# Kernel tuning notes

Measured on AMD Instinct MI355X. Metric: run time of the kernel, lower is better.

Reference implementation:

```python
import jax, jax.numpy as jnp
import numpy as np

N, E, D, H, K = 8192, 8, 1024, 4096, 2


def setup_inputs() -> dict:
    key = jax.random.key(0)
    ks = jax.random.split(key, 12)
    s = 0.02  # init scale for weights
    return {
        "x": jax.random.normal(ks[0], (N, D), jnp.float32),
        "noise": jax.random.normal(ks[1], (N, E), jnp.float32),
        "Wg_w": jax.random.normal(ks[2], (D, E), jnp.float32) * s,
        "Wg_b": jnp.zeros((E,), jnp.float32),
        "Wn_w": jax.random.normal(ks[3], (D, E), jnp.float32) * s,
        "Wn_b": jnp.zeros((E,), jnp.float32),
        "w1": jax.random.normal(ks[4], (E, D, H), jnp.float32) * s,
        "b1": jnp.zeros((E, H), jnp.float32),
        "w2": jax.random.normal(ks[5], (E, H, D), jnp.float32) * s,
        "b2": jnp.zeros((E, D), jnp.float32),
        "k": K,
    }


def reference(x, noise, Wg_w, Wg_b, Wn_w, Wn_b, w1, b1, w2, b2, k):
    # --- noisy top-k gating: H(x) = Wg(x) + noise * softplus(Wn(x)) ---
    g_logits = x @ Wg_w + Wg_b                       # [N, E]
    n_scale = jax.nn.softplus(x @ Wn_w + Wn_b)       # [N, E]
    h = g_logits + noise * n_scale                   # [N, E]
    topk_vals, topk_inds = jax.lax.top_k(h, k)       # [N, k]
    gates = jax.nn.softmax(topk_vals, axis=-1)       # [N, k]

    # Scatter top-k gates into a dense [N, E] map (zeros for unselected experts),
    # so the weighted combine is exactly sum_j gates[n,j] * expert_{inds[n,j]}(x_n).
    n_tok, n_exp = h.shape
    dense_gates = jnp.zeros((n_tok, n_exp), h.dtype).at[
        jnp.arange(n_tok)[:, None], topk_inds
    ].set(gates)                                     # [N, E]

    # --- per-expert 2-layer MLP: fc2(relu(fc1(x))) ---
    hid = jax.nn.relu(jnp.einsum('nd,edh->neh', x, w1) + b1)  # [N, E, H]
    y = jnp.einsum('neh,ehd->ned', hid, w2) + b2              # [N, E, D]
    out = jnp.einsum('ned,ne->nd', y, dense_gates)            # [N, D]
    return out
```

## Files before the change

### kernel.cpp

```cpp
#include <hip/hip_runtime.h>
#include <hip/hip_bf16.h>

#define NTOK 8192
#define NEXP 8
#define DMODEL 1024
#define DHID 4096

typedef __bf16 bf16x8 __attribute__((ext_vector_type(8)));
typedef float f32x4 __attribute__((ext_vector_type(4)));

__device__ __forceinline__ unsigned short f2bf(float f) {
  return __builtin_bit_cast(unsigned short, __float2bfloat16(f));
}

__device__ __forceinline__ void gload_lds16(const void* g, void* l) {
  __builtin_amdgcn_global_load_lds(
      (const __attribute__((address_space(1))) unsigned int*)g,
      (__attribute__((address_space(3))) unsigned int*)l, 16, 0, 0);
}

__device__ __forceinline__ int imin(int a, int b) { return a < b ? a : b; }

constexpr size_t OFF_XB   = 0;
constexpr size_t OFF_W1T  = OFF_XB + (size_t)NTOK * DMODEL * 2;
constexpr size_t OFF_W2T  = OFF_W1T + (size_t)NEXP * DHID * DMODEL * 2;
constexpr size_t OFF_HID  = OFF_W2T + (size_t)NEXP * DMODEL * DHID * 2;
constexpr size_t OFF_IDX  = OFF_HID + (size_t)NTOK * 2 * DHID * 2;
constexpr size_t OFF_GATE = OFF_IDX + (size_t)NTOK * 2 * 4;
constexpr size_t OFF_LIST = OFF_GATE + (size_t)NTOK * 2 * 4;
constexpr size_t OFF_CNT  = OFF_LIST + (size_t)NTOK * 2 * 4;
constexpr size_t OFF_OFFS = OFF_CNT + 128;
constexpr size_t OFF_CUR  = OFF_OFFS + 128;

__global__ __launch_bounds__(256) void prep_kernel(
    const float* __restrict__ w1, const float* __restrict__ w2,
    unsigned short* __restrict__ w1t, unsigned short* __restrict__ w2t,
    const float* __restrict__ x, const float* __restrict__ noise,
    const float* __restrict__ Wg_w, const float* __restrict__ Wg_b,
    const float* __restrict__ Wn_w, const float* __restrict__ Wn_b,
    unsigned short* __restrict__ xb, int* __restrict__ topk_idx,
    float* __restrict__ topk_gate, int* __restrict__ counts) {
  __shared__ float sh[64][65];
  const int bid = blockIdx.x;

  if (bid < 16384) {
    const float* in;
    unsigned short* outp;
    int R, C, r0, c0;
    if (bid < 8192) {
      int e = bid >> 10, rem = bid & 1023;
      R = DMODEL; C = DHID;
      in = w1 + (size_t)e * R * C;
      outp = w1t + (size_t)e * R * C;
      r0 = (rem >> 6) * 64;
      c0 = (rem & 63) * 64;
    } else {
      int t = bid - 8192;
      int e = t >> 10, rem = t & 1023;
      R = DHID; C = DMODEL;
      in = w2 + (size_t)e * R * C;
      outp = w2t + (size_t)e * R * C;
      r0 = (rem >> 4) * 64;
      c0 = (rem & 15) * 64;
    }
    int tx = threadIdx.x & 15, ty = threadIdx.x >> 4;
#pragma unroll
    for (int p = 0; p < 4; ++p) {
      int row = ty + p * 16;
      float4 v = *(const float4*)&in[(size_t)(r0 + row) * C + c0 + tx * 4];
      sh[row][tx * 4 + 0] = v.x;
      sh[row][tx * 4 + 1] = v.y;
      sh[row][tx * 4 + 2] = v.z;
      sh[row][tx * 4 + 3] = v.w;
    }
    __syncthreads();
#pragma unroll
    for (int p = 0; p < 4; ++p) {
      int crow = ty + p * 16;
      ushort4 o;
      o.x = f2bf(sh[tx * 4 + 0][crow]);
      o.y = f2bf(sh[tx * 4 + 1][crow]);
      o.z = f2bf(sh[tx * 4 + 2][crow]);
      o.w = f2bf(sh[tx * 4 + 3][crow]);
      *(ushort4*)&outp[(size_t)(c0 + crow) * R + r0 + tx * 4] = o;
    }
    return;
  }

  int g = bid - 16384;
  int wave = threadIdx.x >> 6;
  int lane = threadIdx.x & 63;
  int n = g * 4 + wave;
  if (n >= NTOK) return;

  float ag[8] = {0.f, 0.f, 0.f, 0.f, 0.f, 0.f, 0.f, 0.f};
  float an[8] = {0.f, 0.f, 0.f, 0.f, 0.f, 0.f, 0.f, 0.f};
  const float* xr = x + (size_t)n * DMODEL;
  unsigned short* xbr = xb + (size_t)n * DMODEL;
#pragma unroll 4
  for (int i = 0; i < DMODEL / 64; ++i) {
    int d = lane + i * 64;
    float xv = xr[d];
    xbr[d] = f2bf(xv);
    const float4* wg = (const float4*)(Wg_w + (size_t)d * 8);
    const float4* wn = (const float4*)(Wn_w + (size_t)d * 8);
    float4 g0 = wg[0], g1 = wg[1];
    float4 n0 = wn[0], n1 = wn[1];
    ag[0] += xv * g0.x; ag[1] += xv * g0.y; ag[2] += xv * g0.z; ag[3] += xv * g0.w;
    ag[4] += xv * g1.x; ag[5] += xv * g1.y; ag[6] += xv * g1.z; ag[7] += xv * g1.w;
    an[0] += xv * n0.x; an[1] += xv * n0.y; an[2] += xv * n0.z; an[3] += xv * n0.w;
    an[4] += xv * n1.x; an[5] += xv * n1.y; an[6] += xv * n1.z; an[7] += xv * n1.w;
  }
#pragma unroll
  for (int off = 32; off > 0; off >>= 1) {
#pragma unroll
    for (int j = 0; j < 8; ++j) {
      ag[j] += __shfl_down(ag[j], off, 64);
      an[j] += __shfl_down(an[j], off, 64);
    }
  }
  if (lane == 0) {
    float h[8];
#pragma unroll
    for (int e = 0; e < 8; ++e) {
      float gl = ag[e] + Wg_b[e];
      float z = an[e] + Wn_b[e];
      float sp = fmaxf(z, 0.f) + log1pf(expf(-fabsf(z)));
      h[e] = gl + noise[(size_t)n * 8 + e] * sp;
    }
    int i0 = 0; float v0 = h[0];
#pragma unroll
    for (int e = 1; e < 8; ++e)
      if (h[e] > v0) { v0 = h[e]; i0 = e; }
    int i1 = -1; float v1 = -1e30f;
#pragma unroll
    for (int e = 0; e < 8; ++e)
      if (e != i0 && h[e] > v1) { v1 = h[e]; i1 = e; }
    float e1 = expf(v1 - v0);
    float inv = 1.f / (1.f + e1);
    topk_idx[n * 2] = i0;
    topk_idx[n * 2 + 1] = i1;
    topk_gate[n * 2] = inv;
    topk_gate[n * 2 + 1] = e1 * inv;
    atomicAdd(&counts[i0], 1);
    atomicAdd(&counts[i1], 1);
  }
}

__global__ void scan_kernel(const int* __restrict__ counts,
                            int* __restrict__ offsets, int* __restrict__ cursor) {
  if (threadIdx.x == 0) {
    int acc = 0;
    for (int e = 0; e < NEXP; ++e) {
      offsets[e] = acc;
      cursor[e] = acc;
      acc += counts[e];
    }
    offsets[NEXP] = acc;
  }
}

__global__ void scatter_kernel(const int* __restrict__ topk_idx,
                               int* __restrict__ cursor, int* __restrict__ list) {
  int n = blockIdx.x * 256 + threadIdx.x;
  if (n >= NTOK) return;
#pragma unroll
  for (int j = 0; j < 2; ++j) {
    int e = topk_idx[n * 2 + j];
    int pos = atomicAdd(&cursor[e], 1);
    list[pos] = n * 2 + j;
  }
}

#define VMW(N) asm volatile("s_waitcnt vmcnt(" #N ")" ::: "memory")

template <int MODE>
__global__ __launch_bounds__(256) void expert_gemm(
    const unsigned short* __restrict__ Asrc, const unsigned short* __restrict__ Bt,
    const float* __restrict__ bias, const int* __restrict__ offsets,
    const int* __restrict__ list, const float* __restrict__ gates,
    unsigned short* __restrict__ hid, float* __restrict__ out) {
  constexpr int Krow = MODE ? DHID : DMODEL;
  constexpr int Nout = MODE ? DMODEL : DHID;
  constexpr int NT = Krow / 64;

  const int gx = gridDim.x, gy = gridDim.y;
  const int lin = blockIdx.x + gx * (blockIdx.y + gy * blockIdx.z);
  const int e = lin & 7;
  int r = lin >> 3;

  int by, bx;
  if (MODE == 0) {
    int st = r >> 6;
    int inner = r & 63;
    int sm = st >> 2, sn = st & 3;
    if (sm & 1) sn = 3 - sn;
    by = sm * 8 + (inner >> 3);
    bx = sn * 8 + (inner & 7);
  } else {
    by = r & 63;
    bx = r >> 6;
  }

  const int off = offsets[e];
  const int ne = offsets[e + 1] - off;
  const int m0 = by * 128;
  if (m0 >= ne) return;
  const int n0 = bx * 128;

  __shared__ alignas(16) unsigned short Al[2][128 * 64];
  __shared__ alignas(16) unsigned short Bl[2][128 * 64];

  const int tid = threadIdx.x;
  const int lane = tid & 63;
  const int w = tid >> 6;
  const int wm = (w >> 1) * 64;
  const int wn = (w & 1) * 64;
  const int lr = lane & 15;
  const int kg = lane >> 4;
  const int ch0 = ((kg ^ (lr & 7)) * 8);
  const int ch1 = (((4 + kg) ^ (lr & 7)) * 8);

  const unsigned short* srcA[4];
  const unsigned short* srcB[4];
#pragma unroll
  for (int i = 0; i < 4; ++i) {
    int q = tid + i * 256;
    int rr = q >> 3, c = q & 7;
    int cs = c ^ (rr & 7);
    int p = off + imin(m0 + rr, ne - 1);
    if (MODE == 0) {
      int token = list[p] >> 1;
      srcA[i] = Asrc + (size_t)token * DMODEL + cs * 8;
    } else {
      srcA[i] = Asrc + (size_t)p * DHID + cs * 8;
    }
    srcB[i] = Bt + (size_t)e * Nout * Krow + (size_t)(n0 + rr) * Krow + cs * 8;
  }

  f32x4 acc[4][4] = {};

  auto stage = [&](int slot, int kt) {
#pragma unroll
    for (int i = 0; i < 4; ++i) {
      int q = tid + i * 256;
      gload_lds16(srcA[i] + kt * 64, &Al[slot][q * 8]);
      gload_lds16(srcB[i] + kt * 64, &Bl[slot][q * 8]);
    }
  };

  auto compute = [&](int slot) {
    bf16x8 af[4][2], bfr[4][2];
#pragma unroll
    for (int mf = 0; mf < 4; ++mf) {
      const unsigned short* base = &Al[slot][(wm + mf * 16 + lr) * 64];
      af[mf][0] = *(const bf16x8*)(base + ch0);
      af[mf][1] = *(const bf16x8*)(base + ch1);
    }
#pragma unroll
    for (int nf = 0; nf < 4; ++nf) {
      const unsigned short* base = &Bl[slot][(wn + nf * 16 + lr) * 64];
      bfr[nf][0] = *(const bf16x8*)(base + ch0);
      bfr[nf][1] = *(const bf16x8*)(base + ch1);
    }
    asm volatile("s_waitcnt lgkmcnt(0)" ::: "memory");
    __builtin_amdgcn_sched_barrier(0);
#pragma unroll
    for (int kk = 0; kk < 2; ++kk)
#pragma unroll
      for (int mf = 0; mf < 4; ++mf)
#pragma unroll
        for (int nf = 0; nf < 4; ++nf)
          acc[mf][nf] = __builtin_amdgcn_mfma_f32_16x16x32_bf16(
              af[mf][kk], bfr[nf][kk], acc[mf][nf], 0, 0, 0);
  };

  stage(0, 0);
  stage(1, 1);

  int cur = 0;
  for (int t = 0; t < NT; ++t) {
    if (t < NT - 1) { VMW(8); }
    else { VMW(0); }
    __builtin_amdgcn_s_barrier();
    __builtin_amdgcn_sched_barrier(0);
    compute(cur);
    asm volatile("s_waitcnt lgkmcnt(0)" ::: "memory");
    __builtin_amdgcn_sched_barrier(0);
    __builtin_amdgcn_s_barrier();
    if (t + 2 < NT) stage(cur, t + 2);
    cur ^= 1;
  }

  if (MODE == 0) {
#pragma unroll
    for (int mf = 0; mf < 4; ++mf) {
#pragma unroll
      for (int j = 0; j < 4; ++j) {
        int rloc = wm + mf * 16 + kg * 4 + j;
        int row = m0 + rloc;
        if (row < ne) {
          size_t p = (size_t)(off + row);
#pragma unroll
          for (int nf = 0; nf < 4; ++nf) {
            int col = n0 + wn + nf * 16 + lr;
            float v = acc[mf][nf][j] + bias[(size_t)e * Nout + col];
            hid[p * DHID + col] = f2bf(fmaxf(v, 0.f));
          }
        }
      }
    }
  } else {
#pragma unroll
    for (int mf = 0; mf < 4; ++mf) {
#pragma unroll
      for (int j = 0; j < 4; ++j) {
        int rloc = wm + mf * 16 + kg * 4 + j;
        int row = m0 + rloc;
        if (row < ne) {
          int lv = list[off + row];
          int token = lv >> 1;
          float g = gates[lv];
#pragma unroll
          for (int nf = 0; nf < 4; ++nf) {
            int col = n0 + wn + nf * 16 + lr;
            float v = (acc[mf][nf][j] + bias[(size_t)e * Nout + col]) * g;
            atomicAdd(&out[(size_t)token * DMODEL + col], v);
          }
        }
      }
    }
  }
}

extern "C" void kernel_launch(void* const* d_in, const int* in_sizes, int n_in,
                              void* d_out, int out_size, void* d_ws, size_t ws_size,
                              hipStream_t stream) {
  const float* x = (const float*)d_in[0];
  const float* noise = (const float*)d_in[1];
  const float* Wg_w = (const float*)d_in[2];
  const float* Wg_b = (const float*)d_in[3];
  const float* Wn_w = (const float*)d_in[4];
  const float* Wn_b = (const float*)d_in[5];
  const float* w1 = (const float*)d_in[6];
  const float* b1 = (const float*)d_in[7];
  const float* w2 = (const float*)d_in[8];
  const float* b2 = (const float*)d_in[9];
  float* out = (float*)d_out;

  char* ws = (char*)d_ws;
  unsigned short* xb = (unsigned short*)(ws + OFF_XB);
  unsigned short* w1t = (unsigned short*)(ws + OFF_W1T);
  unsigned short* w2t = (unsigned short*)(ws + OFF_W2T);
  unsigned short* hid = (unsigned short*)(ws + OFF_HID);
  int* topk_idx = (int*)(ws + OFF_IDX);
  float* topk_gate = (float*)(ws + OFF_GATE);
  int* list = (int*)(ws + OFF_LIST);
  int* counts = (int*)(ws + OFF_CNT);
  int* offsets = (int*)(ws + OFF_OFFS);
  int* cursor = (int*)(ws + OFF_CUR);

  hipMemsetAsync(out, 0, (size_t)NTOK * DMODEL * sizeof(float), stream);
  hipMemsetAsync(counts, 0, NEXP * sizeof(int), stream);

  prep_kernel<<<18432, 256, 0, stream>>>(w1, w2, w1t, w2t, x, noise, Wg_w, Wg_b,
                                         Wn_w, Wn_b, xb, topk_idx, topk_gate,
                                         counts);
  scan_kernel<<<1, 64, 0, stream>>>(counts, offsets, cursor);
  scatter_kernel<<<NTOK / 256, 256, 0, stream>>>(topk_idx, cursor, list);

  expert_gemm<0><<<dim3(32, 64, NEXP), 256, 0, stream>>>(
      xb, w1t, b1, offsets, list, topk_gate, hid, nullptr);
  expert_gemm<1><<<dim3(8, 64, NEXP), 256, 0, stream>>>(
      hid, w2t, b2, offsets, list, topk_gate, nullptr, out);
}
```

Measured before the change: 904.4 us.

## Switch expert GEMM to triple-buffered BK=32 pipeline with occupancy hint

Halves the K tile from 64 to 32 and uses three LDS buffers instead of two, so the kernel prefetches two tiles ahead while using less shared memory (48KB vs 64KB). It re-derives the LDS XOR swizzle for 32-wide rows, adds a launch-bounds occupancy hint of 4 blocks per CU, and raises wave priority around the MFMA block in the second GEMM. The intent is deeper latency hiding and higher occupancy. In exchange the kernel runs twice as many barrier-synchronised iterations with less MFMA work between each pair of barriers, and register pressure may become a constraint under the occupancy hint.

```diff
diff --git a/kernel.cpp b/kernel.cpp
--- a/kernel.cpp
+++ b/kernel.cpp
@@ -175,14 +175,14 @@
 #define VMW(N) asm volatile("s_waitcnt vmcnt(" #N ")" ::: "memory")
 
 template <int MODE>
-__global__ __launch_bounds__(256) void expert_gemm(
+__global__ __launch_bounds__(256, 4) void expert_gemm(
     const unsigned short* __restrict__ Asrc, const unsigned short* __restrict__ Bt,
     const float* __restrict__ bias, const int* __restrict__ offsets,
     const int* __restrict__ list, const float* __restrict__ gates,
     unsigned short* __restrict__ hid, float* __restrict__ out) {
   constexpr int Krow = MODE ? DHID : DMODEL;
   constexpr int Nout = MODE ? DMODEL : DHID;
-  constexpr int NT = Krow / 64;
+  constexpr int NT = Krow / 32;
 
   const int gx = gridDim.x, gy = gridDim.y;
   const int lin = blockIdx.x + gx * (blockIdx.y + gy * blockIdx.z);
@@ -208,8 +208,8 @@
   if (m0 >= ne) return;
   const int n0 = bx * 128;
 
-  __shared__ alignas(16) unsigned short Al[2][128 * 64];
-  __shared__ alignas(16) unsigned short Bl[2][128 * 64];
+  __shared__ alignas(16) unsigned short Al[3][128 * 32];
+  __shared__ alignas(16) unsigned short Bl[3][128 * 32];
 
   const int tid = threadIdx.x;
   const int lane = tid & 63;
@@ -218,16 +218,15 @@
   const int wn = (w & 1) * 64;
   const int lr = lane & 15;
   const int kg = lane >> 4;
-  const int ch0 = ((kg ^ (lr & 7)) * 8);
-  const int ch1 = (((4 + kg) ^ (lr & 7)) * 8);
-
-  const unsigned short* srcA[4];
-  const unsigned short* srcB[4];
-#pragma unroll
-  for (int i = 0; i < 4; ++i) {
+  const int chrd = (kg ^ ((lr >> 1) & 3)) * 8;
+
+  const unsigned short* srcA[2];
+  const unsigned short* srcB[2];
+#pragma unroll
+  for (int i = 0; i < 2; ++i) {
     int q = tid + i * 256;
-    int rr = q >> 3, c = q & 7;
-    int cs = c ^ (rr & 7);
+    int rr = q >> 2, c = q & 3;
+    int cs = c ^ ((rr >> 1) & 3);
     int p = off + imin(m0 + rr, ne - 1);
     if (MODE == 0) {
       int token = list[p] >> 1;
@@ -242,45 +241,41 @@
 
   auto stage = [&](int slot, int kt) {
 #pragma unroll
-    for (int i = 0; i < 4; ++i) {
+    for (int i = 0; i < 2; ++i) {
       int q = tid + i * 256;
-      gload_lds16(srcA[i] + kt * 64, &Al[slot][q * 8]);
-      gload_lds16(srcB[i] + kt * 64, &Bl[slot][q * 8]);
+      gload_lds16(srcA[i] + kt * 32, &Al[slot][q * 8]);
+      gload_lds16(srcB[i] + kt * 32, &Bl[slot][q * 8]);
     }
   };
 
   auto compute = [&](int slot) {
-    bf16x8 af[4][2], bfr[4][2];
-#pragma unroll
-    for (int mf = 0; mf < 4; ++mf) {
-      const unsigned short* base = &Al[slot][(wm + mf * 16 + lr) * 64];
-      af[mf][0] = *(const bf16x8*)(base + ch0);
-      af[mf][1] = *(const bf16x8*)(base + ch1);
-    }
-#pragma unroll
-    for (int nf = 0; nf < 4; ++nf) {
-      const unsigned short* base = &Bl[slot][(wn + nf * 16 + lr) * 64];
-      bfr[nf][0] = *(const bf16x8*)(base + ch0);
-      bfr[nf][1] = *(const bf16x8*)(base + ch1);
-    }
+    bf16x8 af[4], bfr[4];
+#pragma unroll
+    for (int mf = 0; mf < 4; ++mf)
+      af[mf] = *(const bf16x8*)&Al[slot][(wm + mf * 16 + lr) * 32 + chrd];
+#pragma unroll
+    for (int nf = 0; nf < 4; ++nf)
+      bfr[nf] = *(const bf16x8*)&Bl[slot][(wn + nf * 16 + lr) * 32 + chrd];
     asm volatile("s_waitcnt lgkmcnt(0)" ::: "memory");
     __builtin_amdgcn_sched_barrier(0);
-#pragma unroll
-    for (int kk = 0; kk < 2; ++kk)
-#pragma unroll
-      for (int mf = 0; mf < 4; ++mf)
-#pragma unroll
-        for (int nf = 0; nf < 4; ++nf)
-          acc[mf][nf] = __builtin_amdgcn_mfma_f32_16x16x32_bf16(
-              af[mf][kk], bfr[nf][kk], acc[mf][nf], 0, 0, 0);
+    if (MODE == 1) __builtin_amdgcn_s_setprio(1);
+#pragma unroll
+    for (int mf = 0; mf < 4; ++mf)
+#pragma unroll
+      for (int nf = 0; nf < 4; ++nf)
+        acc[mf][nf] = __builtin_amdgcn_mfma_f32_16x16x32_bf16(af[mf], bfr[nf],
+                                                              acc[mf][nf], 0, 0, 0);
+    if (MODE == 1) __builtin_amdgcn_s_setprio(0);
   };
 
   stage(0, 0);
   stage(1, 1);
+  stage(2, 2);
 
   int cur = 0;
   for (int t = 0; t < NT; ++t) {
-    if (t < NT - 1) { VMW(8); }
+    if (t < NT - 2) { VMW(8); }
+    else if (t == NT - 2) { VMW(4); }
     else { VMW(0); }
     __builtin_amdgcn_s_barrier();
     __builtin_amdgcn_sched_barrier(0);
@@ -288,8 +283,8 @@
     asm volatile("s_waitcnt lgkmcnt(0)" ::: "memory");
     __builtin_amdgcn_sched_barrier(0);
     __builtin_amdgcn_s_barrier();
-    if (t + 2 < NT) stage(cur, t + 2);
-    cur ^= 1;
+    if (t + 3 < NT) stage(cur, t + 3);
+    cur = (cur == 2) ? 0 : cur + 1;
   }
 
   if (MODE == 0) {
```

Result: faster. 829.5 us (-8.3%).
